# Kernel optimization log

Hardware: AMD Instinct MI355X
Metric: run time of the kernel (lower is better)

## Reference

```python
import jax, jax.numpy as jnp
import numpy as np

WINDOW_SYNC = 20   # min(20, T//2) with T=8192
WINDOW_SURGE = 10
BN_EPS = 1e-5      # BatchNorm1d eval-mode, running_mean=0, running_var=1


def _corr_matrix(x):
    # x: [w, A] observations x variables -> [A, A] Pearson correlation
    xc = x - x.mean(0)
    cov = xc.T @ xc
    d = jnp.sqrt(jnp.diag(cov))
    return cov / (d[:, None] * d[None, :])


def _offdiag_mean(C):
    A = C.shape[0]
    return (C.sum() - jnp.trace(C)) / (A * (A - 1))


def _rolling_offdiag_corr(returns, window):
    # mean off-diagonal correlation over each trailing window [i-window, i)
    T, A = returns.shape
    starts = jnp.arange(T - window)
    def one(s):
        w = jax.lax.dynamic_slice(returns, (s, 0), (window, A))
        return _offdiag_mean(_corr_matrix(w))
    return jax.vmap(one)(starts)


def setup_inputs() -> dict:
    key = jax.random.key(0)
    ks = jax.random.split(key, 10)
    T, A, H = 8192, 128, 128
    returns_sequence = jax.random.normal(ks[0], (T, A), dtype=jnp.float32) * 0.02
    positions = jax.random.normal(ks[1], (A,), dtype=jnp.float32)
    s1 = 1.0 / np.sqrt(2 * A)
    s2 = 1.0 / np.sqrt(H)
    s3 = 1.0 / np.sqrt(H // 2)
    return {
        "returns_sequence": returns_sequence,
        "positions": positions,
        "w1": jax.random.uniform(ks[2], (2 * A, H), jnp.float32, -s1, s1),
        "b1": jax.random.uniform(ks[3], (H,), jnp.float32, -s1, s1),
        "gamma": jnp.ones((H,), jnp.float32),
        "beta": jnp.zeros((H,), jnp.float32),
        "w2": jax.random.uniform(ks[4], (H, H // 2), jnp.float32, -s2, s2),
        "b2": jax.random.uniform(ks[5], (H // 2,), jnp.float32, -s2, s2),
        "w3": jax.random.uniform(ks[6], (H // 2, 3), jnp.float32, -s3, s3),
        "b3": jax.random.uniform(ks[7], (3,), jnp.float32, -s3, s3),
    }


def reference(returns_sequence, positions, w1, b1, gamma, beta, w2, b2, w3, b3):
    returns = returns_sequence
    T, A = returns.shape

    # ---- herding index ----
    cs_std = jnp.std(returns, axis=1, ddof=1)                 # [T]
    herding_trend = -jnp.diff(cs_std).mean()
    avg_dispersion = cs_std.mean()
    herding_index = jnp.clip(herding_trend / (avg_dispersion + 1e-6) + 0.5, 0.0, 1.0)

    # ---- synchronization ----
    corr = _corr_matrix(returns)                              # [A, A]
    avg_correlation = _offdiag_mean(corr)
    rolling = _rolling_offdiag_corr(returns, WINDOW_SYNC)     # [T-20]
    phase_locking = (rolling > 0.7).astype(jnp.float32).mean()
    eigvals = jnp.linalg.eigvalsh(corr)
    sync_indicator = eigvals.max() / A
    sync_risk = jnp.minimum(1.0, sync_indicator * avg_correlation)

    # ---- diversity loss ----
    return_diversity = 1.0 - jnp.abs(corr).mean()             # includes diagonal (as in torch)
    pa = jnp.abs(positions)
    position_diversity = 1.0 - (pa / pa.sum()).max()
    diversity_loss = 1.0 - jnp.sqrt(return_diversity * position_diversity)

    # ---- correlation surge ----
    rolling10 = _rolling_offdiag_corr(returns, WINDOW_SURGE)  # [T-10]
    recent = rolling10[-5:].mean()
    historical = rolling10[:-5].mean()
    surge_raw = jnp.clip((recent - historical) / historical, 0.0, 1.0)
    correlation_surge = jnp.where(historical > 0, surge_raw, 0.0)

    # ---- phase coupling (pairwise sign concordance) ----
    signs = jnp.sign(returns)                                 # [T, A]
    classes = jnp.array([-1.0, 0.0, 1.0], dtype=returns.dtype)
    I = (signs[None, :, :] == classes[:, None, None]).astype(returns.dtype)  # [3, T, A]
    M = jnp.einsum('cta,ctb->ab', I, I) / T                   # eq-fraction matrix [A, A]
    avg_concordance = _offdiag_mean(M)
    phase_coupling = jnp.clip((avg_concordance - 0.5) * 2.0, 0.0, 1.0)

    # ---- herding detector MLP (BatchNorm1d in eval mode) ----
    feats = jnp.concatenate([returns[-1], positions])         # [2A]
    h = jax.nn.relu(feats @ w1 + b1)
    h = gamma * (h / jnp.sqrt(1.0 + BN_EPS)) + beta
    h = jax.nn.relu(h @ w2 + b2)
    logits = h @ w3 + b3
    herding_severity = jax.nn.softmax(logits)[2]

    collective_risk = (herding_index + sync_risk + diversity_loss) / 3.0

    return jnp.stack([herding_index, herding_severity, sync_risk, phase_locking,
                      diversity_loss, correlation_surge, phase_coupling, collective_risk])
```

## Files before the change

kernel.cpp:

```cpp
#include <hip/hip_runtime.h>
#include <math.h>

#define TN 8192
#define AN 128
#define NW20 (TN - 20)
#define NW10 (TN - 10)

#define NB_GRAM 128
#define NB_ROW  512
#define NB_R20  511
#define NB_R10  512
#define NB_WORK (NB_GRAM + NB_ROW + NB_R20 + NB_R10)

#define WS_STD0 0
#define WS_STDL 1
#define WS_SEV  7
#define WS_SPEC 8
#define WS_BLK  200
#define WS_PAS  3600
#define WS_PAM  3601
#define WS_DEND 4096

template <int W>
__device__ __forceinline__ void roll_strip4(const float* __restrict__ x,
                                            int s0, int nwin, int lane,
                                            double& accA, double& accB) {
  constexpr int NR = W + 3;
  float a0[NR], a1[NR];
#pragma unroll
  for (int t = 0; t < NR; ++t) {
    int r = s0 + t; r = (r < TN) ? r : (TN - 1);
    float2 v = *(const float2*)(x + (size_t)r * AN + 2 * lane);
    a0[t] = v.x; a1[t] = v.y;
  }
#pragma unroll
  for (int w4 = 0; w4 < 4; ++w4) {
    int s = s0 + w4;
    if (s < nwin) {
      float sf0 = 0.f, sf1 = 0.f;
#pragma unroll
      for (int t = 0; t < W; ++t) { sf0 += a0[w4 + t]; sf1 += a1[w4 + t]; }
      float mu0 = sf0 / W, mu1 = sf1 / W;
      float v0 = 0.f, v1 = 0.f;
#pragma unroll
      for (int t = 0; t < W; ++t) {
        float d0 = a0[w4 + t] - mu0, d1 = a1[w4 + t] - mu1;
        v0 += d0 * d0; v1 += d1 * d1;
      }
      float i0 = 1.0f / sqrtf(v0), i1 = 1.0f / sqrtf(v1);
      float q[W];
#pragma unroll
      for (int t = 0; t < W; ++t)
        q[t] = (a0[w4 + t] - mu0) * i0 + (a1[w4 + t] - mu1) * i1;
      int n = W;
#pragma unroll
      for (int o = 1; o <= 32; o <<= 1) {
#pragma unroll
        for (int k = 0; k < n; ++k) q[k] += __shfl_xor(q[k], o);
        if (n > 1) {
          int nh = n >> 1;
          bool hi = (lane & o) != 0;
#pragma unroll
          for (int k = 0; k < nh; ++k) q[k] = hi ? q[2 * k + 1] : q[2 * k];
          if (n & 1) { q[nh] = q[2 * nh]; n = nh + 1; } else { n = nh; }
        }
      }
      float alpha = (W == 20) ? ((lane & 16) ? 0.125f : 0.5f)
                              : ((lane & 8) ? 0.0625f : 0.25f);
      float r = q[0] * q[0] * alpha;
#pragma unroll
      for (int o = 32; o; o >>= 1) r += __shfl_xor(r, o);
      if (lane == 0) {
        double off = ((double)r - (double)AN) / ((double)AN * (AN - 1));
        if (W == 20) {
          accA += (off > 0.7) ? 1.0 : 0.0;
        } else {
          accA += off;
          if (s >= TN - W - 5) accB += off;
        }
      }
    }
  }
}

__global__ void __launch_bounds__(256) k_main(const float* __restrict__ x,
                                              double* __restrict__ wsd,
                                              float* __restrict__ pc,
                                              float* __restrict__ pdg,
                                              float* __restrict__ pg) {
  __shared__ union {
    float stage[8][AN];
    double tacc[4][2];
  } sm;
  const int b = blockIdx.x;
  const int tid = threadIdx.x;
  const int lane = tid & 63;
  const int w = tid >> 6;

  if (b < NB_GRAM) {
    int i0 = (tid >> 4) * 8;
    int j0 = (tid & 15) * 8;
    int lrow = tid >> 5;
    int lcol = (tid & 31) * 4;
    const float* xs = x + (size_t)b * 64 * AN;
    float acc[8][8];
#pragma unroll
    for (int a = 0; a < 8; ++a)
#pragma unroll
      for (int c = 0; c < 8; ++c) acc[a][c] = 0.f;
    float4 v = *(const float4*)(xs + lrow * AN + lcol);
    for (int it = 0; it < 8; ++it) {
      __syncthreads();
      *(float4*)(&sm.stage[lrow][lcol]) = v;
      __syncthreads();
      if (it + 1 < 8)
        v = *(const float4*)(xs + ((it + 1) * 8 + lrow) * AN + lcol);
#pragma unroll
      for (int r = 0; r < 8; ++r) {
        float aa[8], bb[8];
        *(float4*)(aa) = *(const float4*)(&sm.stage[r][i0]);
        *(float4*)(aa + 4) = *(const float4*)(&sm.stage[r][i0 + 4]);
        *(float4*)(bb) = *(const float4*)(&sm.stage[r][j0]);
        *(float4*)(bb + 4) = *(const float4*)(&sm.stage[r][j0 + 4]);
#pragma unroll
        for (int ai = 0; ai < 8; ++ai)
#pragma unroll
          for (int bj = 0; bj < 8; ++bj)
            acc[ai][bj] = fmaf(aa[ai], bb[bj], acc[ai][bj]);
      }
    }
    float* dst = pg + (size_t)b * (AN * AN);
#pragma unroll
    for (int ai = 0; ai < 8; ++ai)
#pragma unroll
      for (int bj = 0; bj < 8; bj += 4)
        *(float4*)(dst + (i0 + ai) * AN + j0 + bj) =
            make_float4(acc[ai][bj], acc[ai][bj + 1], acc[ai][bj + 2],
                        acc[ai][bj + 3]);
    if ((tid >> 4) == (tid & 15)) {
#pragma unroll
      for (int k = 0; k < 8; ++k) pdg[b * AN + i0 + k] = acc[k][k];
    }
    if (tid < AN) {
      float cs = 0.f;
      for (int r = 0; r < 64; ++r) cs += xs[r * AN + tid];
      pc[b * AN + tid] = cs;
    }
    return;
  }

  if (b < NB_GRAM + NB_ROW) {
    int rb = b - NB_GRAM;
    double sstd = 0.0, sconc = 0.0;
    for (int rr = 0; rr < 4; ++rr) {
      int t = rb * 16 + w * 4 + rr;
      float2 xv = *(const float2*)(x + (size_t)t * AN + 2 * lane);
      float x0 = xv.x, x1 = xv.y;
      float s = x0 + x1;
#pragma unroll
      for (int o = 32; o; o >>= 1) s += __shfl_xor(s, o);
      float mean = s * (1.0f / AN);
      float d0 = x0 - mean, d1 = x1 - mean;
      float q = d0 * d0 + d1 * d1;
#pragma unroll
      for (int o = 32; o; o >>= 1) q += __shfl_xor(q, o);
      float sd = sqrtf(q / (float)(AN - 1));
      int pk = (int)(x0 < 0.f) + (int)(x1 < 0.f)
             + (((int)(x0 == 0.f) + (int)(x1 == 0.f)) << 10)
             + (((int)(x0 > 0.f) + (int)(x1 > 0.f)) << 20);
#pragma unroll
      for (int o = 32; o; o >>= 1) pk += __shfl_xor(pk, o);
      if (lane == 0) {
        int nn = pk & 1023, nz = (pk >> 10) & 1023, np = (pk >> 20) & 1023;
        sconc += (double)nn * nn + (double)nz * nz + (double)np * np;
        sstd += (double)sd;
        if (t == 0) wsd[WS_STD0] = (double)sd;
        if (t == TN - 1) wsd[WS_STDL] = (double)sd;
      }
    }
    if (lane == 0) { sm.tacc[w][0] = sstd; sm.tacc[w][1] = sconc; }
    __syncthreads();
    if (tid == 0) {
      wsd[WS_BLK + (size_t)b * 2 + 0] =
          sm.tacc[0][0] + sm.tacc[1][0] + sm.tacc[2][0] + sm.tacc[3][0];
      wsd[WS_BLK + (size_t)b * 2 + 1] =
          sm.tacc[0][1] + sm.tacc[1][1] + sm.tacc[2][1] + sm.tacc[3][1];
    }
    return;
  }

  if (b < NB_GRAM + NB_ROW + NB_R20) {
    int s0 = (b - (NB_GRAM + NB_ROW)) * 16 + w * 4;
    double cnt = 0.0, dummy = 0.0;
    roll_strip4<20>(x, s0, NW20, lane, cnt, dummy);
    if (lane == 0) { sm.tacc[w][0] = cnt; }
    __syncthreads();
    if (tid == 0)
      wsd[WS_BLK + (size_t)b * 2 + 0] =
          sm.tacc[0][0] + sm.tacc[1][0] + sm.tacc[2][0] + sm.tacc[3][0];
    return;
  }

  {
    int s0 = (b - (NB_GRAM + NB_ROW + NB_R20)) * 16 + w * 4;
    double s10 = 0.0, s10l5 = 0.0;
    roll_strip4<10>(x, s0, NW10, lane, s10, s10l5);
    if (lane == 0) { sm.tacc[w][0] = s10; sm.tacc[w][1] = s10l5; }
    __syncthreads();
    if (tid == 0) {
      wsd[WS_BLK + (size_t)b * 2 + 0] =
          sm.tacc[0][0] + sm.tacc[1][0] + sm.tacc[2][0] + sm.tacc[3][0];
      wsd[WS_BLK + (size_t)b * 2 + 1] =
          sm.tacc[0][1] + sm.tacc[1][1] + sm.tacc[2][1] + sm.tacc[3][1];
    }
  }
}

__global__ void __launch_bounds__(256) k_fold(
    const float* __restrict__ pc, const float* __restrict__ pdg,
    const float* __restrict__ pg, double* __restrict__ wsd,
    float* __restrict__ corr, const float* __restrict__ x,
    const float* __restrict__ pos, const float* __restrict__ w1,
    const float* __restrict__ b1, const float* __restrict__ gamma,
    const float* __restrict__ beta, const float* __restrict__ w2,
    const float* __restrict__ b2, const float* __restrict__ w3,
    const float* __restrict__ b3) {
  __shared__ double r0[256], r1[256], r2[256], r3[256], r4[256];
  int b = blockIdx.x;
  int t = threadIdx.x;
  int lane = t & 63;
  int w = t >> 6;
  if (b < 64) {
    __shared__ double muS[AN], dS[AN], csP[AN], dgP[AN];
    if (t < AN) {
      double cs = 0.0;
#pragma unroll 16
      for (int s = 0; s < NB_GRAM; ++s) cs += (double)pc[s * AN + t];
      csP[t] = cs;
    } else {
      int u = t - AN;
      double dg = 0.0;
#pragma unroll 16
      for (int s = 0; s < NB_GRAM; ++s) dg += (double)pdg[s * AN + u];
      dgP[u] = dg;
    }
    __syncthreads();
    if (t < AN) {
      double mu = csP[t] / (double)TN;
      muS[t] = mu;
      dS[t] = sqrt(dgP[t] - (double)TN * mu * mu);
    }
    __syncthreads();
    int e = b * 256 + t;
    int i = e >> 7, j = e & (AN - 1);
    double cv = 0.0;
#pragma unroll 16
    for (int s = 0; s < NB_GRAM; ++s) cv += (double)pg[(size_t)s * (AN * AN) + e];
    cv -= (double)TN * muS[i] * muS[j];
    double c = cv / (dS[i] * dS[j]);
    corr[e] = (float)c;
    r0[t] = c;
    r1[t] = fabs(c);
    r2[t] = (i == j) ? c : 0.0;
    __syncthreads();
    for (int sft = 128; sft; sft >>= 1) {
      if (t < sft) { r0[t] += r0[t + sft]; r1[t] += r1[t + sft]; r2[t] += r2[t + sft]; }
      __syncthreads();
    }
    if (t == 0) {
      wsd[WS_SPEC + b * 3 + 0] = r0[0];
      wsd[WS_SPEC + b * 3 + 1] = r1[0];
      wsd[WS_SPEC + b * 3 + 2] = r2[0];
    }
    return;
  }

  __shared__ float f[2 * AN], prt[256], h1[AN], h2[64], lg[3];
  __shared__ double pr2[4];
  {
    double a = 0.0, bc = 0.0, cnt = 0.0, s10 = 0.0, s10l5 = 0.0;
    for (int k = NB_GRAM + t; k < NB_WORK; k += 256) {
      const double* p = wsd + WS_BLK + (size_t)k * 2;
      if (k < NB_GRAM + NB_ROW) { a += p[0]; bc += p[1]; }
      else if (k < NB_GRAM + NB_ROW + NB_R20) cnt += p[0];
      else { s10 += p[0]; s10l5 += p[1]; }
    }
    r0[t] = a; r1[t] = bc; r2[t] = cnt; r3[t] = s10; r4[t] = s10l5;
    __syncthreads();
    for (int sft = 128; sft; sft >>= 1) {
      if (t < sft) {
        r0[t] += r0[t + sft]; r1[t] += r1[t + sft]; r2[t] += r2[t + sft];
        r3[t] += r3[t + sft]; r4[t] += r4[t + sft];
      }
      __syncthreads();
    }
    if (t == 0) {
      wsd[2] = r0[0];
      wsd[3] = r1[0];
      wsd[4] = r2[0];
      wsd[5] = r3[0];
      wsd[6] = r4[0];
    }
  }
  f[t] = (t < AN) ? x[(size_t)(TN - 1) * AN + t] : pos[t - AN];
  __syncthreads();
  {
    int n = t & 127, h = t >> 7;
    float acc = 0.f;
    const float* wcol = w1 + h * 128 * AN + n;
    const float* fv = f + h * 128;
    for (int k = 0; k < 128; ++k) acc = fmaf(fv[k], wcol[k * AN], acc);
    prt[t] = acc;
  }
  __syncthreads();
  if (t < AN) {
    float acc = b1[t] + prt[t] + prt[t + 128];
    acc = fmaxf(acc, 0.0f);
    h1[t] = gamma[t] * (acc / sqrtf(1.0f + 1e-5f)) + beta[t];
  }
  __syncthreads();
  if (t < 64) {
    float acc = b2[t];
    for (int k = 0; k < AN; ++k) acc = fmaf(h1[k], w2[k * 64 + t], acc);
    h2[t] = fmaxf(acc, 0.0f);
  }
  __syncthreads();
  if (t < 3) {
    float acc = b3[t];
    for (int k = 0; k < 64; ++k) acc = fmaf(h2[k], w3[k * 3 + t], acc);
    lg[t] = acc;
  }
  if (t < AN) {
    double pa = fabs((double)pos[t]);
    double ps = pa, pm = pa;
#pragma unroll
    for (int o = 32; o; o >>= 1) {
      ps += __shfl_xor(ps, o);
      pm = fmax(pm, __shfl_xor(pm, o));
    }
    if (lane == 0) { pr2[w] = ps; pr2[2 + w] = pm; }
  }
  __syncthreads();
  if (t == 0) {
    float m = fmaxf(lg[0], fmaxf(lg[1], lg[2]));
    float e0 = expf(lg[0] - m), e1 = expf(lg[1] - m), e2 = expf(lg[2] - m);
    wsd[WS_SEV] = (double)(e2 / (e0 + e1 + e2));
    wsd[WS_PAS] = pr2[0] + pr2[1];
    wsd[WS_PAM] = fmax(pr2[2], pr2[3]);
  }
}

__global__ void __launch_bounds__(256) k_spec_tail(
    const double* __restrict__ wsd, const float* __restrict__ corr,
    float* __restrict__ out) {
  __shared__ float vv[AN], prt[256], un[AN], red[4];
  __shared__ double spec[3];
  int t = threadIdx.x;
  int lane = t & 63;
  int w = t >> 6;
  int c = t & (AN - 1), hh = t >> 7;
  const float* cp = corr + (size_t)hh * 64 * AN + c;
  float creg[64];
#pragma unroll
  for (int k = 0; k < 64; ++k) creg[k] = cp[(size_t)k * AN];
  if (t < 64) {
    double s0 = wsd[WS_SPEC + t * 3 + 0];
    double s1 = wsd[WS_SPEC + t * 3 + 1];
    double s2 = wsd[WS_SPEC + t * 3 + 2];
#pragma unroll
    for (int o = 32; o; o >>= 1) {
      s0 += __shfl_xor(s0, o);
      s1 += __shfl_xor(s1, o);
      s2 += __shfl_xor(s2, o);
    }
    if (t == 0) { spec[0] = s0; spec[1] = s1; spec[2] = s2; }
  }
  if (t < AN) vv[t] = 1.0f;
  __syncthreads();
  float lam = 0.0f;
  for (int it = 0; it < 12; ++it) {
    float acc = 0.f;
#pragma unroll
    for (int k = 0; k < 64; ++k)
      acc = fmaf(creg[k], vv[hh * 64 + k], acc);
    prt[t] = acc;
    __syncthreads();
    if (t < AN) {
      float u = prt[t] + prt[t + 128];
      un[t] = u;
      float sq = u * u;
#pragma unroll
      for (int o = 32; o; o >>= 1) sq += __shfl_xor(sq, o);
      if (lane == 0) red[w] = sq;
    }
    __syncthreads();
    lam = sqrtf(red[0] + red[1]);
    if (t < AN) vv[t] = un[t] / lam;
    __syncthreads();
  }
  if (t != 0) return;
  double sev = wsd[WS_SEV];
  double sumstd = wsd[2], conc = wsd[3], cnt20 = wsd[4];
  double sum10 = wsd[5], sum10l5 = wsd[6];
  double avg_disp = sumstd / (double)TN;
  double trend = -(wsd[WS_STDL] - wsd[WS_STD0]) / (double)(TN - 1);
  double hi = trend / (avg_disp + 1e-6) + 0.5;
  hi = fmin(1.0, fmax(0.0, hi));
  double avg_corr = (spec[0] - spec[2]) / ((double)AN * (AN - 1));
  double sync_ind = (double)lam / (double)AN;
  double sync_risk = fmin(1.0, sync_ind * avg_corr);
  double pl = cnt20 / (double)(TN - 20);
  double rd = 1.0 - spec[1] / ((double)AN * AN);
  double pd = 1.0 - wsd[WS_PAM] / wsd[WS_PAS];
  double dl = 1.0 - sqrt(rd * pd);
  double recent = sum10l5 / 5.0;
  double hist = (sum10 - sum10l5) / (double)(TN - 10 - 5);
  double sraw = (recent - hist) / hist;
  sraw = fmin(1.0, fmax(0.0, sraw));
  double surge = (hist > 0.0) ? sraw : 0.0;
  double ac = (conc / (double)TN - (double)AN) / ((double)AN * (AN - 1));
  double pcup = fmin(1.0, fmax(0.0, (ac - 0.5) * 2.0));
  double cr = (hi + sync_risk + dl) / 3.0;
  out[0] = (float)hi;
  out[1] = (float)sev;
  out[2] = (float)sync_risk;
  out[3] = (float)pl;
  out[4] = (float)dl;
  out[5] = (float)surge;
  out[6] = (float)pcup;
  out[7] = (float)cr;
}

extern "C" void kernel_launch(void* const* d_in, const int* in_sizes, int n_in,
                              void* d_out, int out_size, void* d_ws, size_t ws_size,
                              hipStream_t stream) {
  const float* x     = (const float*)d_in[0];
  const float* pos   = (const float*)d_in[1];
  const float* w1    = (const float*)d_in[2];
  const float* b1    = (const float*)d_in[3];
  const float* gamma = (const float*)d_in[4];
  const float* beta  = (const float*)d_in[5];
  const float* w2    = (const float*)d_in[6];
  const float* b2    = (const float*)d_in[7];
  const float* w3    = (const float*)d_in[8];
  const float* b3    = (const float*)d_in[9];
  float* out = (float*)d_out;
  double* wsd = (double*)d_ws;
  float* corr = (float*)(wsd + WS_DEND);
  float* pc   = corr + AN * AN;
  float* pdg  = pc + NB_GRAM * AN;
  float* pg   = pdg + NB_GRAM * AN;

  k_main<<<NB_WORK, 256, 0, stream>>>(x, wsd, pc, pdg, pg);
  k_fold<<<65, 256, 0, stream>>>(pc, pdg, pg, wsd, corr, x, pos, w1, b1,
                                 gamma, beta, w2, b2, w3, b3);
  k_spec_tail<<<1, 256, 0, stream>>>(wsd, corr, out);
}
```

Baseline: 114.6 us.

## Fuse per-row stats into rolling-20 blocks and split Gram fold across 128 blocks

Removes the separate 512 row-statistics blocks by computing cross-sectional std and sign-concordance inside the rolling-20 correlation blocks, reusing the rows already loaded into registers. The fold kernel now uses 128 blocks, one per correlation row, and each thread sums half of the Gram partials, replacing 64 blocks that each summed all 128 partials per element. The workspace layout and the spectral reduction are adjusted to match. This cuts redundant global loads and block count, but adds register pressure to the fused rolling blocks.

```diff
diff --git a/kernel.cpp b/kernel.cpp
--- a/kernel.cpp
+++ b/kernel.cpp
@@ -7,19 +7,18 @@
 #define NW10 (TN - 10)
 
 #define NB_GRAM 128
-#define NB_ROW  512
-#define NB_R20  511
+#define NB_R20  512
 #define NB_R10  512
-#define NB_WORK (NB_GRAM + NB_ROW + NB_R20 + NB_R10)
+#define NB_WORK (NB_GRAM + NB_R20 + NB_R10)
 
 #define WS_STD0 0
 #define WS_STDL 1
 #define WS_SEV  7
 #define WS_SPEC 8
-#define WS_BLK  200
-#define WS_PAS  3600
-#define WS_PAM  3601
-#define WS_DEND 4096
+#define WS_PAS  396
+#define WS_PAM  397
+#define WS_BLK  400
+#define WS_DEND 8192
 
 template <int W>
 __device__ __forceinline__ void roll_strip4(const float* __restrict__ x,
@@ -83,6 +82,89 @@
   }
 }
 
+__device__ __forceinline__ void roll20_stats(const float* __restrict__ x,
+                                             int s0, int lane,
+                                             double* __restrict__ wsd,
+                                             double& cnt, double& sstd,
+                                             double& sconc) {
+  constexpr int W = 20, NR = 23;
+  float a0[NR], a1[NR];
+#pragma unroll
+  for (int t = 0; t < NR; ++t) {
+    int r = s0 + t; r = (r < TN) ? r : (TN - 1);
+    float2 v = *(const float2*)(x + (size_t)r * AN + 2 * lane);
+    a0[t] = v.x; a1[t] = v.y;
+  }
+#pragma unroll
+  for (int rr = 0; rr < 4; ++rr) {
+    int t = s0 + rr;
+    float x0 = a0[rr], x1 = a1[rr];
+    float s = x0 + x1;
+#pragma unroll
+    for (int o = 32; o; o >>= 1) s += __shfl_xor(s, o);
+    float mean = s * (1.0f / AN);
+    float d0 = x0 - mean, d1 = x1 - mean;
+    float q = d0 * d0 + d1 * d1;
+#pragma unroll
+    for (int o = 32; o; o >>= 1) q += __shfl_xor(q, o);
+    float sd = sqrtf(q / (float)(AN - 1));
+    int pk = (int)(x0 < 0.f) + (int)(x1 < 0.f)
+           + (((int)(x0 == 0.f) + (int)(x1 == 0.f)) << 10)
+           + (((int)(x0 > 0.f) + (int)(x1 > 0.f)) << 20);
+#pragma unroll
+    for (int o = 32; o; o >>= 1) pk += __shfl_xor(pk, o);
+    if (lane == 0) {
+      int nn = pk & 1023, nz = (pk >> 10) & 1023, np = (pk >> 20) & 1023;
+      sconc += (double)nn * nn + (double)nz * nz + (double)np * np;
+      sstd += (double)sd;
+      if (t == 0) wsd[WS_STD0] = (double)sd;
+      if (t == TN - 1) wsd[WS_STDL] = (double)sd;
+    }
+  }
+#pragma unroll
+  for (int w4 = 0; w4 < 4; ++w4) {
+    int s = s0 + w4;
+    if (s < NW20) {
+      float sf0 = 0.f, sf1 = 0.f;
+#pragma unroll
+      for (int t = 0; t < W; ++t) { sf0 += a0[w4 + t]; sf1 += a1[w4 + t]; }
+      float mu0 = sf0 / W, mu1 = sf1 / W;
+      float v0 = 0.f, v1 = 0.f;
+#pragma unroll
+      for (int t = 0; t < W; ++t) {
+        float d0 = a0[w4 + t] - mu0, d1 = a1[w4 + t] - mu1;
+        v0 += d0 * d0; v1 += d1 * d1;
+      }
+      float i0 = 1.0f / sqrtf(v0), i1 = 1.0f / sqrtf(v1);
+      float q[W];
+#pragma unroll
+      for (int t = 0; t < W; ++t)
+        q[t] = (a0[w4 + t] - mu0) * i0 + (a1[w4 + t] - mu1) * i1;
+      int n = W;
+#pragma unroll
+      for (int o = 1; o <= 32; o <<= 1) {
+#pragma unroll
+        for (int k = 0; k < n; ++k) q[k] += __shfl_xor(q[k], o);
+        if (n > 1) {
+          int nh = n >> 1;
+          bool hi = (lane & o) != 0;
+#pragma unroll
+          for (int k = 0; k < nh; ++k) q[k] = hi ? q[2 * k + 1] : q[2 * k];
+          if (n & 1) { q[nh] = q[2 * nh]; n = nh + 1; } else { n = nh; }
+        }
+      }
+      float alpha = (lane & 16) ? 0.125f : 0.5f;
+      float r = q[0] * q[0] * alpha;
+#pragma unroll
+      for (int o = 32; o; o >>= 1) r += __shfl_xor(r, o);
+      if (lane == 0) {
+        double off = ((double)r - (double)AN) / ((double)AN * (AN - 1));
+        cnt += (off > 0.7) ? 1.0 : 0.0;
+      }
+    }
+  }
+}
+
 __global__ void __launch_bounds__(256) k_main(const float* __restrict__ x,
                                               double* __restrict__ wsd,
                                               float* __restrict__ pc,
@@ -90,7 +172,7 @@
                                               float* __restrict__ pg) {
   __shared__ union {
     float stage[8][AN];
-    double tacc[4][2];
+    double tacc[4][3];
   } sm;
   const int b = blockIdx.x;
   const int tid = threadIdx.x;
@@ -149,68 +231,35 @@
     return;
   }
 
-  if (b < NB_GRAM + NB_ROW) {
-    int rb = b - NB_GRAM;
-    double sstd = 0.0, sconc = 0.0;
-    for (int rr = 0; rr < 4; ++rr) {
-      int t = rb * 16 + w * 4 + rr;
-      float2 xv = *(const float2*)(x + (size_t)t * AN + 2 * lane);
-      float x0 = xv.x, x1 = xv.y;
-      float s = x0 + x1;
-#pragma unroll
-      for (int o = 32; o; o >>= 1) s += __shfl_xor(s, o);
-      float mean = s * (1.0f / AN);
-      float d0 = x0 - mean, d1 = x1 - mean;
-      float q = d0 * d0 + d1 * d1;
-#pragma unroll
-      for (int o = 32; o; o >>= 1) q += __shfl_xor(q, o);
-      float sd = sqrtf(q / (float)(AN - 1));
-      int pk = (int)(x0 < 0.f) + (int)(x1 < 0.f)
-             + (((int)(x0 == 0.f) + (int)(x1 == 0.f)) << 10)
-             + (((int)(x0 > 0.f) + (int)(x1 > 0.f)) << 20);
-#pragma unroll
-      for (int o = 32; o; o >>= 1) pk += __shfl_xor(pk, o);
-      if (lane == 0) {
-        int nn = pk & 1023, nz = (pk >> 10) & 1023, np = (pk >> 20) & 1023;
-        sconc += (double)nn * nn + (double)nz * nz + (double)np * np;
-        sstd += (double)sd;
-        if (t == 0) wsd[WS_STD0] = (double)sd;
-        if (t == TN - 1) wsd[WS_STDL] = (double)sd;
-      }
-    }
-    if (lane == 0) { sm.tacc[w][0] = sstd; sm.tacc[w][1] = sconc; }
+  if (b < NB_GRAM + NB_R20) {
+    int s0 = (b - NB_GRAM) * 16 + w * 4;
+    double cnt = 0.0, sstd = 0.0, sconc = 0.0;
+    roll20_stats(x, s0, lane, wsd, cnt, sstd, sconc);
+    if (lane == 0) {
+      sm.tacc[w][0] = cnt; sm.tacc[w][1] = sstd; sm.tacc[w][2] = sconc;
+    }
     __syncthreads();
     if (tid == 0) {
-      wsd[WS_BLK + (size_t)b * 2 + 0] =
+      wsd[WS_BLK + (size_t)b * 4 + 0] =
           sm.tacc[0][0] + sm.tacc[1][0] + sm.tacc[2][0] + sm.tacc[3][0];
-      wsd[WS_BLK + (size_t)b * 2 + 1] =
+      wsd[WS_BLK + (size_t)b * 4 + 1] =
           sm.tacc[0][1] + sm.tacc[1][1] + sm.tacc[2][1] + sm.tacc[3][1];
+      wsd[WS_BLK + (size_t)b * 4 + 2] =
+          sm.tacc[0][2] + sm.tacc[1][2] + sm.tacc[2][2] + sm.tacc[3][2];
     }
     return;
   }
 
-  if (b < NB_GRAM + NB_ROW + NB_R20) {
-    int s0 = (b - (NB_GRAM + NB_ROW)) * 16 + w * 4;
-    double cnt = 0.0, dummy = 0.0;
-    roll_strip4<20>(x, s0, NW20, lane, cnt, dummy);
-    if (lane == 0) { sm.tacc[w][0] = cnt; }
-    __syncthreads();
-    if (tid == 0)
-      wsd[WS_BLK + (size_t)b * 2 + 0] =
-          sm.tacc[0][0] + sm.tacc[1][0] + sm.tacc[2][0] + sm.tacc[3][0];
-    return;
-  }
-
   {
-    int s0 = (b - (NB_GRAM + NB_ROW + NB_R20)) * 16 + w * 4;
+    int s0 = (b - (NB_GRAM + NB_R20)) * 16 + w * 4;
     double s10 = 0.0, s10l5 = 0.0;
     roll_strip4<10>(x, s0, NW10, lane, s10, s10l5);
     if (lane == 0) { sm.tacc[w][0] = s10; sm.tacc[w][1] = s10l5; }
     __syncthreads();
     if (tid == 0) {
-      wsd[WS_BLK + (size_t)b * 2 + 0] =
+      wsd[WS_BLK + (size_t)b * 4 + 0] =
           sm.tacc[0][0] + sm.tacc[1][0] + sm.tacc[2][0] + sm.tacc[3][0];
-      wsd[WS_BLK + (size_t)b * 2 + 1] =
+      wsd[WS_BLK + (size_t)b * 4 + 1] =
           sm.tacc[0][1] + sm.tacc[1][1] + sm.tacc[2][1] + sm.tacc[3][1];
     }
   }
@@ -230,8 +279,13 @@
   int t = threadIdx.x;
   int lane = t & 63;
   int w = t >> 6;
-  if (b < 64) {
-    __shared__ double muS[AN], dS[AN], csP[AN], dgP[AN];
+  if (b < 128) {
+    __shared__ double muS[AN], dS[AN], csP[AN], dgP[AN], part[256];
+    int j = t & 127, half = t >> 7;
+    double cvp = 0.0;
+    const float* pgp = pg + (size_t)(half * 64) * (AN * AN) + b * AN + j;
+#pragma unroll 16
+    for (int s = 0; s < 64; ++s) cvp += (double)pgp[(size_t)s * (AN * AN)];
     if (t < AN) {
       double cs = 0.0;
 #pragma unroll 16
@@ -244,6 +298,7 @@
       for (int s = 0; s < NB_GRAM; ++s) dg += (double)pdg[s * AN + u];
       dgP[u] = dg;
     }
+    part[t] = cvp;
     __syncthreads();
     if (t < AN) {
       double mu = csP[t] / (double)TN;
@@ -251,17 +306,17 @@
       dS[t] = sqrt(dgP[t] - (double)TN * mu * mu);
     }
     __syncthreads();
-    int e = b * 256 + t;
-    int i = e >> 7, j = e & (AN - 1);
-    double cv = 0.0;
-#pragma unroll 16
-    for (int s = 0; s < NB_GRAM; ++s) cv += (double)pg[(size_t)s * (AN * AN) + e];
-    cv -= (double)TN * muS[i] * muS[j];
-    double c = cv / (dS[i] * dS[j]);
-    corr[e] = (float)c;
-    r0[t] = c;
-    r1[t] = fabs(c);
-    r2[t] = (i == j) ? c : 0.0;
+    if (t < 128) {
+      double cv = part[t] + part[t + 128];
+      cv -= (double)TN * muS[b] * muS[t];
+      double c = cv / (dS[b] * dS[t]);
+      corr[b * AN + t] = (float)c;
+      r0[t] = c;
+      r1[t] = fabs(c);
+      r2[t] = (t == b) ? c : 0.0;
+    } else {
+      r0[t] = 0.0; r1[t] = 0.0; r2[t] = 0.0;
+    }
     __syncthreads();
     for (int sft = 128; sft; sft >>= 1) {
       if (t < sft) { r0[t] += r0[t + sft]; r1[t] += r1[t + sft]; r2[t] += r2[t + sft]; }
@@ -278,14 +333,13 @@
   __shared__ float f[2 * AN], prt[256], h1[AN], h2[64], lg[3];
   __shared__ double pr2[4];
   {
-    double a = 0.0, bc = 0.0, cnt = 0.0, s10 = 0.0, s10l5 = 0.0;
+    double cnt = 0.0, sstd = 0.0, sconc = 0.0, s10 = 0.0, s10l5 = 0.0;
     for (int k = NB_GRAM + t; k < NB_WORK; k += 256) {
-      const double* p = wsd + WS_BLK + (size_t)k * 2;
-      if (k < NB_GRAM + NB_ROW) { a += p[0]; bc += p[1]; }
-      else if (k < NB_GRAM + NB_ROW + NB_R20) cnt += p[0];
+      const double* p = wsd + WS_BLK + (size_t)k * 4;
+      if (k < NB_GRAM + NB_R20) { cnt += p[0]; sstd += p[1]; sconc += p[2]; }
       else { s10 += p[0]; s10l5 += p[1]; }
     }
-    r0[t] = a; r1[t] = bc; r2[t] = cnt; r3[t] = s10; r4[t] = s10l5;
+    r0[t] = sstd; r1[t] = sconc; r2[t] = cnt; r3[t] = s10; r4[t] = s10l5;
     __syncthreads();
     for (int sft = 128; sft; sft >>= 1) {
       if (t < sft) {
@@ -354,7 +408,7 @@
     const double* __restrict__ wsd, const float* __restrict__ corr,
     float* __restrict__ out) {
   __shared__ float vv[AN], prt[256], un[AN], red[4];
-  __shared__ double spec[3];
+  __shared__ double specW[2][3];
   int t = threadIdx.x;
   int lane = t & 63;
   int w = t >> 6;
@@ -363,7 +417,7 @@
   float creg[64];
 #pragma unroll
   for (int k = 0; k < 64; ++k) creg[k] = cp[(size_t)k * AN];
-  if (t < 64) {
+  if (t < 128) {
     double s0 = wsd[WS_SPEC + t * 3 + 0];
     double s1 = wsd[WS_SPEC + t * 3 + 1];
     double s2 = wsd[WS_SPEC + t * 3 + 2];
@@ -373,7 +427,7 @@
       s1 += __shfl_xor(s1, o);
       s2 += __shfl_xor(s2, o);
     }
-    if (t == 0) { spec[0] = s0; spec[1] = s1; spec[2] = s2; }
+    if (lane == 0) { specW[w][0] = s0; specW[w][1] = s1; specW[w][2] = s2; }
   }
   if (t < AN) vv[t] = 1.0f;
   __syncthreads();
@@ -399,6 +453,9 @@
     __syncthreads();
   }
   if (t != 0) return;
+  double spec0 = specW[0][0] + specW[1][0];
+  double spec1 = specW[0][1] + specW[1][1];
+  double spec2 = specW[0][2] + specW[1][2];
   double sev = wsd[WS_SEV];
   double sumstd = wsd[2], conc = wsd[3], cnt20 = wsd[4];
   double sum10 = wsd[5], sum10l5 = wsd[6];
@@ -406,11 +463,11 @@
   double trend = -(wsd[WS_STDL] - wsd[WS_STD0]) / (double)(TN - 1);
   double hi = trend / (avg_disp + 1e-6) + 0.5;
   hi = fmin(1.0, fmax(0.0, hi));
-  double avg_corr = (spec[0] - spec[2]) / ((double)AN * (AN - 1));
+  double avg_corr = (spec0 - spec2) / ((double)AN * (AN - 1));
   double sync_ind = (double)lam / (double)AN;
   double sync_risk = fmin(1.0, sync_ind * avg_corr);
   double pl = cnt20 / (double)(TN - 20);
-  double rd = 1.0 - spec[1] / ((double)AN * AN);
+  double rd = 1.0 - spec1 / ((double)AN * AN);
   double pd = 1.0 - wsd[WS_PAM] / wsd[WS_PAS];
   double dl = 1.0 - sqrt(rd * pd);
   double recent = sum10l5 / 5.0;
@@ -452,7 +509,7 @@
   float* pg   = pdg + NB_GRAM * AN;
 
   k_main<<<NB_WORK, 256, 0, stream>>>(x, wsd, pc, pdg, pg);
-  k_fold<<<65, 256, 0, stream>>>(pc, pdg, pg, wsd, corr, x, pos, w1, b1,
-                                 gamma, beta, w2, b2, w3, b3);
+  k_fold<<<129, 256, 0, stream>>>(pc, pdg, pg, wsd, corr, x, pos, w1, b1,
+                                  gamma, beta, w2, b2, w3, b3);
   k_spec_tail<<<1, 256, 0, stream>>>(wsd, corr, out);
 }
```

Result: no change. 114.4 us (-0.2%).
